# Performance work log

Measured on AMD Instinct MI355X. Metric: run time of the kernel, lower is better.

The kernel has to match this reference:

```python
import jax, jax.numpy as jnp
import numpy as np

N_NODES = 100000
N_EDGES = 1600000
IN_DIM, HID_DIM, OUT_DIM = 128, 128, 64


def setup_inputs() -> dict:
    key = jax.random.key(0)
    ks = jax.random.split(key, 8)
    x = jax.random.normal(ks[0], (N_NODES, IN_DIM), dtype=jnp.float32)
    edge_index = jax.random.randint(ks[1], (2, N_EDGES), 0, N_NODES, dtype=jnp.int64)
    s1 = 1.0 / np.sqrt(IN_DIM)
    s2 = 1.0 / np.sqrt(HID_DIM)
    return {
        "x": x,
        "edge_index": edge_index,
        "W1l": jax.random.normal(ks[2], (IN_DIM, HID_DIM), dtype=jnp.float32) * s1,
        "b1": jnp.zeros((HID_DIM,), dtype=jnp.float32),
        "W1r": jax.random.normal(ks[3], (IN_DIM, HID_DIM), dtype=jnp.float32) * s1,
        "W2l": jax.random.normal(ks[4], (HID_DIM, OUT_DIM), dtype=jnp.float32) * s2,
        "b2": jnp.zeros((OUT_DIM,), dtype=jnp.float32),
        "W2r": jax.random.normal(ks[5], (HID_DIM, OUT_DIM), dtype=jnp.float32) * s2,
    }


def _sage_conv(h, src, dst, n_nodes, Wl, bl, Wr):
    # mean-aggregate neighbor messages src -> dst, then linear + root linear
    msg = h[src]                                               # [E, d]
    summed = jax.ops.segment_sum(msg, dst, num_segments=n_nodes)
    cnt = jax.ops.segment_sum(jnp.ones((src.shape[0],), h.dtype), dst,
                              num_segments=n_nodes)
    aggr = summed / jnp.maximum(cnt, 1.0)[:, None]             # [N, d]
    return aggr @ Wl + bl + h @ Wr                             # [N, d_out]


def reference(x, edge_index, W1l, b1, W1r, W2l, b2, W2r):
    src, dst = edge_index[0], edge_index[1]
    n = x.shape[0]
    h = jax.nn.relu(_sage_conv(x, src, dst, n, W1l, b1, W1r))
    # dropout is identity in eval mode (training=False)
    return _sage_conv(h, src, dst, n, W2l, b2, W2r)
```

## Files before the change

### kernel.cpp

```cpp
#include <hip/hip_runtime.h>
#include <hip/hip_bf16.h>
#include <stdint.h>

#define N_NODES 100000
#define N_EDGES 1600000
#define IN_DIM 128
#define HID_DIM 128
#define OUT_DIM 64
#define NBUCKET 391
#define NBE 391
#define ECHUNK 4096
#define HM (NBUCKET * NBE)
#define NB_SCAN 150
#define SENTINEL N_NODES
#define PCAP 6144
#define GEMM_ROWBLKS 782

typedef __bf16 bf16x8 __attribute__((ext_vector_type(8)));
typedef float f32x4 __attribute__((ext_vector_type(4)));
typedef float f32x2 __attribute__((ext_vector_type(2)));

__device__ __forceinline__ uint16_t f_to_bf16(float f) {
    uint32_t u = __float_as_uint(f);
    u += 0x7fffu + ((u >> 16) & 1u);
    return (uint16_t)(u >> 16);
}
__device__ __forceinline__ uint32_t pack_bf16x2(float lo, float hi) {
    return (uint32_t)f_to_bf16(lo) | ((uint32_t)f_to_bf16(hi) << 16);
}


__global__ __launch_bounds__(256) void prep_k(const int* __restrict__ dst,
                                              const float* __restrict__ x,
                                              const float* __restrict__ W1l,
                                              const float* __restrict__ W1r,
                                              const float* __restrict__ W2l,
                                              const float* __restrict__ W2r,
                                              int* __restrict__ hist,
                                              uint32_t* __restrict__ xf8,
                                              uint16_t* __restrict__ wT1,
                                              uint16_t* __restrict__ wT2) {
    __shared__ int lh[NBUCKET];
    int blk = blockIdx.x, t = threadIdx.x;
    if (blk < NBE) {
        for (int i = t; i < NBUCKET; i += 256) lh[i] = 0;
        __syncthreads();
        int e0 = blk * ECHUNK;
        int e1 = e0 + ECHUNK; if (e1 > N_EDGES) e1 = N_EDGES;
        for (int e = e0 + t; e < e1; e += 256) atomicAdd(&lh[dst[e] >> 8], 1);
        __syncthreads();
        for (int i = t; i < NBUCKET; i += 256) hist[i * NBE + blk] = lh[i];
    } else if (blk < NBE + 6250) {
        int i = (blk - NBE) * 256 + t;
        if (blk == NBE && t < 32) xf8[N_NODES * 32 + t] = 0u;
        if (i >= N_NODES * IN_DIM / 8) return;
        const float4* xv = (const float4*)x;
        float4 v0 = xv[2 * i], v1 = xv[2 * i + 1];
        int p0 = __builtin_amdgcn_cvt_pk_fp8_f32(v0.x, v0.y, 0, false);
        p0 = __builtin_amdgcn_cvt_pk_fp8_f32(v0.z, v0.w, p0, true);
        int p1 = __builtin_amdgcn_cvt_pk_fp8_f32(v1.x, v1.y, 0, false);
        p1 = __builtin_amdgcn_cvt_pk_fp8_f32(v1.z, v1.w, p1, true);
        uint2 w2; w2.x = (uint32_t)p0; w2.y = (uint32_t)p1;
        ((uint2*)xf8)[i] = w2;
    } else {
        int i = (blk - NBE - 6250) * 256 + t;
        if (i < 128 * 256) {
            int n = i >> 8, k = i & 255;
            float v = (k < 128) ? W1l[k * 128 + n] : W1r[(k - 128) * 128 + n];
            wT1[i] = f_to_bf16(v);
        } else {
            int j = i - 128 * 256;
            if (j < 128 * 128) {
                int n = j >> 7, k = j & 127;
                float v = (n < 64) ? W2l[k * 64 + n] : W2r[k * 64 + (n - 64)];
                wT2[j] = f_to_bf16(v);
            }
        }
    }
}


__global__ void scan1_k(int* __restrict__ data, int* __restrict__ partials, int n) {
    __shared__ int sm[256];
    int tid = threadIdx.x;
    int base = blockIdx.x * 1024 + tid * 4;
    int v0 = 0, v1 = 0, v2 = 0, v3 = 0;
    if (base + 0 < n) v0 = data[base + 0];
    if (base + 1 < n) v1 = data[base + 1];
    if (base + 2 < n) v2 = data[base + 2];
    if (base + 3 < n) v3 = data[base + 3];
    int tot = v0 + v1 + v2 + v3;
    sm[tid] = tot;
    __syncthreads();
    int val = tot;
    for (int off = 1; off < 256; off <<= 1) {
        int x = (tid >= off) ? sm[tid - off] : 0;
        __syncthreads();
        val += x;
        sm[tid] = val;
        __syncthreads();
    }
    int excl = val - tot;
    if (tid == 255) partials[blockIdx.x] = val;
    if (base + 0 < n) data[base + 0] = excl;
    if (base + 1 < n) data[base + 1] = excl + v0;
    if (base + 2 < n) data[base + 2] = excl + v0 + v1;
    if (base + 3 < n) data[base + 3] = excl + v0 + v1 + v2;
}

__global__ void scan3_k(int* __restrict__ data, const int* __restrict__ partials, int n) {
    __shared__ int sm[256];
    __shared__ int sp[256];
    int t = threadIdx.x;
    int v = (t < NB_SCAN) ? partials[t] : 0;
    sm[t] = v;
    __syncthreads();
    int val = v;
    for (int off = 1; off < 256; off <<= 1) {
        int x = (t >= off) ? sm[t - off] : 0;
        __syncthreads();
        val += x;
        sm[t] = val;
        __syncthreads();
    }
    sp[t] = val - v;
    __syncthreads();
    int i = blockIdx.x * 256 + t;
    if (i < n) data[i] += sp[i >> 10];
}

__global__ __launch_bounds__(256) void scatter2_k(const int* __restrict__ src,
                                                  const int* __restrict__ dst,
                                                  const int* __restrict__ hoff,
                                                  uint32_t* __restrict__ packed) {
    __shared__ int loff[NBUCKET];
    int blk = blockIdx.x, t = threadIdx.x;
    for (int i = t; i < NBUCKET; i += 256) loff[i] = hoff[i * NBE + blk];
    __syncthreads();
    int e0 = blk * ECHUNK;
    int e1 = e0 + ECHUNK; if (e1 > N_EDGES) e1 = N_EDGES;
    for (int e = e0 + t; e < e1; e += 256) {
        int d = dst[e];
        int pos = atomicAdd(&loff[d >> 8], 1);
        packed[pos] = ((uint32_t)src[e] << 8) | (uint32_t)(d & 255);
    }
}


__global__ __launch_bounds__(256) void finalize_k(const uint32_t* __restrict__ packed,
                                                  const int* __restrict__ hoff,
                                                  int* __restrict__ csr,
                                                  int* __restrict__ deg,
                                                  int* __restrict__ prowst) {
    __shared__ int lhist[256];
    __shared__ int ssc[256];
    __shared__ int lcur[256];
    __shared__ int s_pcnt;
    __shared__ uint32_t lpk[PCAP];
    __shared__ int lcsr[PCAP];
    int b = blockIdx.x, t = threadIdx.x;
    int base = hoff[b * NBE];
    int next = (b + 1 < NBUCKET) ? hoff[(b + 1) * NBE] : N_EDGES;
    int cnt = next - base;
    lhist[t] = 0;
    __syncthreads();
    bool fit = (cnt <= PCAP);
    if (fit) {
        for (int i = t; i < cnt; i += 256) {
            uint32_t pk = packed[base + i];
            lpk[i] = pk;
            atomicAdd(&lhist[pk & 255u], 1);
        }
    } else {
        for (int i = t; i < cnt; i += 256) atomicAdd(&lhist[packed[base + i] & 255u], 1);
    }
    __syncthreads();
    int d = lhist[t];
    int pd = (d + 7) & ~7;
    ssc[t] = pd;
    __syncthreads();
    int val = pd;
    for (int off = 1; off < 256; off <<= 1) {
        int x = (t >= off) ? ssc[t - off] : 0;
        __syncthreads();
        val += x;
        ssc[t] = val;
        __syncthreads();
    }
    int excl = val - pd;
    lcur[t] = excl;
    if (t == 255) s_pcnt = val;
    int node = (b << 8) + t;
    if (node < N_NODES) { deg[node] = d; prowst[node] = b * PCAP + excl; }
    __syncthreads();
    int pcnt = s_pcnt;
    int cbase = b * PCAP;
    if (fit && pcnt <= PCAP) {
        for (int i = t; i < pcnt; i += 256) lcsr[i] = SENTINEL;
        __syncthreads();
        for (int i = t; i < cnt; i += 256) {
            uint32_t pk = lpk[i];
            int pos = atomicAdd(&lcur[pk & 255u], 1);
            lcsr[pos] = (int)(pk >> 8);
        }
        __syncthreads();
        for (int i = t; i < pcnt; i += 256) csr[cbase + i] = lcsr[i];
    } else {
        int lim = pcnt < PCAP ? pcnt : PCAP;
        for (int i = t; i < lim; i += 256) csr[cbase + i] = SENTINEL;
        __syncthreads();
        for (int i = t; i < cnt; i += 256) {
            uint32_t pk = packed[base + i];
            int pos = atomicAdd(&lcur[pk & 255u], 1);
            if (pos < PCAP) csr[cbase + pos] = (int)(pk >> 8);
        }
    }
}


__global__ void aggregate_k(const int* __restrict__ csr, const int* __restrict__ prowst,
                            const int* __restrict__ deg,
                            const uint32_t* __restrict__ inf8, uint32_t* __restrict__ out2) {
    int gw = (blockIdx.x * blockDim.x + threadIdx.x) >> 6;
    int lane = threadIdx.x & 63;
    int c = lane & 31, p = lane >> 5;
    int node = 2 * gw + p;
    int start = prowst[node];
    int d = deg[node];
    int pd = (d + 7) & ~7;
    f32x2 s01 = (f32x2){0.f, 0.f}, s23 = (f32x2){0.f, 0.f};
    for (int j = 0; j < pd; j += 8) {
        uint32_t q[8];
#pragma unroll
        for (int u = 0; u < 8; u++) {
            int s = csr[start + j + u];
            q[u] = inf8[(s << 5) + c];
        }
#pragma unroll
        for (int u = 0; u < 8; u++) {
            s01 += __builtin_amdgcn_cvt_pk_f32_fp8((int)q[u], false);
            s23 += __builtin_amdgcn_cvt_pk_f32_fp8((int)q[u], true);
        }
    }
    float inv = 1.0f / (float)(d > 0 ? d : 1);
    uint2 o;
    o.x = pack_bf16x2(s01[0] * inv, s01[1] * inv);
    o.y = pack_bf16x2(s23[0] * inv, s23[1] * inv);
    ((uint2*)out2)[node * 32 + c] = o;
}


__global__ __launch_bounds__(256, 2) void gemm12_k(const uint16_t* __restrict__ ab,
                                                   const float* __restrict__ x,
                                                   const uint16_t* __restrict__ wT1,
                                                   const float* __restrict__ b1,
                                                   const uint16_t* __restrict__ wT2,
                                                   const float* __restrict__ b2,
                                                   uint8_t* __restrict__ g,
                                                   float* __restrict__ z) {
    __shared__ uint16_t lwA[64 * 256];
    __shared__ uint16_t lhb[128 * 128];
    int t = threadIdx.x;
    int rowblk = blockIdx.x;
    if (rowblk == 0 && t < 16)
        ((uint32_t*)(g + (size_t)N_NODES * 64))[t] = 0u;

    int wave = t >> 6;
    int lane = t & 63;
    int m0 = rowblk * 128 + wave * 32;
    int mr = lane & 15, quad = lane >> 4;

    const uint16_t* A1[2];
    const float* A2[2];
#pragma unroll
    for (int s = 0; s < 2; s++) {
        int row = m0 + s * 16 + mr;
        if (row > N_NODES - 1) row = N_NODES - 1;
        A1[s] = ab + (size_t)row * 128 + quad * 8;
        A2[s] = x + (size_t)row * 128 + quad * 8;
    }

    for (int nh = 0; nh < 2; nh++) {
        {
            const uint4* gsrc = (const uint4*)wT1;
            uint4* ldst = (uint4*)lwA;
            for (int i = t; i < 2048; i += 256) {
                int r = i >> 5, cc = i & 31;
                ldst[(r << 5) + (cc ^ (r & 31))] = gsrc[((nh * 64 + r) << 5) + cc];
            }
        }
        __syncthreads();

        f32x4 acc[4][2];
#pragma unroll
        for (int nt = 0; nt < 4; nt++)
#pragma unroll
            for (int s = 0; s < 2; s++) acc[nt][s] = (f32x4){0.f, 0.f, 0.f, 0.f};

#pragma unroll
        for (int kt = 0; kt < 8; kt++) {
            bf16x8 av[2];
#pragma unroll
            for (int s = 0; s < 2; s++) {
                if (kt < 4) {
                    av[s] = *reinterpret_cast<const bf16x8*>(A1[s] + kt * 32);
                } else {
                    const float* ap = A2[s] + (kt - 4) * 32;
                    float4 f0 = *reinterpret_cast<const float4*>(ap);
                    float4 f1 = *reinterpret_cast<const float4*>(ap + 4);
                    union { uint16_t u[8]; bf16x8 v; } cv;
                    cv.u[0] = f_to_bf16(f0.x); cv.u[1] = f_to_bf16(f0.y);
                    cv.u[2] = f_to_bf16(f0.z); cv.u[3] = f_to_bf16(f0.w);
                    cv.u[4] = f_to_bf16(f1.x); cv.u[5] = f_to_bf16(f1.y);
                    cv.u[6] = f_to_bf16(f1.z); cv.u[7] = f_to_bf16(f1.w);
                    av[s] = cv.v;
                }
            }
#pragma unroll
            for (int nt = 0; nt < 4; nt++) {
                int brow = nt * 16 + mr;
                int chunk = kt * 4 + quad;
                const uint16_t* bp = lwA + (brow << 8) + ((chunk ^ (brow & 31)) << 3);
                bf16x8 b = *reinterpret_cast<const bf16x8*>(bp);
#pragma unroll
                for (int s = 0; s < 2; s++)
                    acc[nt][s] = __builtin_amdgcn_mfma_f32_16x16x32_bf16(av[s], b, acc[nt][s], 0, 0, 0);
            }
        }
        __syncthreads();

#pragma unroll
        for (int nt = 0; nt < 4; nt++) {
            int col = nh * 64 + nt * 16 + mr;
            float bias = b1[col];
            int c2 = col >> 3, clo = col & 7;
#pragma unroll
            for (int s = 0; s < 2; s++) {
#pragma unroll
                for (int r = 0; r < 4; r++) {
                    int lrow = wave * 32 + s * 16 + quad * 4 + r;
                    float v = acc[nt][s][r] + bias;
                    v = v > 0.f ? v : 0.f;
                    lhb[(lrow << 7) + ((c2 ^ (lrow & 15)) << 3) + clo] = f_to_bf16(v);
                }
            }
        }
    }

    {
        const uint4* gsrc = (const uint4*)wT2;
        uint4* ldst = (uint4*)lwA;
        for (int i = t; i < 2048; i += 256) {
            int r = i >> 4, cc = i & 15;
            ldst[(r << 4) + (cc ^ (r & 15))] = gsrc[(r << 4) + cc];
        }
    }
    __syncthreads();

    f32x4 acc2[8][2];
#pragma unroll
    for (int nt = 0; nt < 8; nt++)
#pragma unroll
        for (int s = 0; s < 2; s++) acc2[nt][s] = (f32x4){0.f, 0.f, 0.f, 0.f};

#pragma unroll
    for (int kt = 0; kt < 4; kt++) {
        bf16x8 av[2];
#pragma unroll
        for (int s = 0; s < 2; s++) {
            int row = wave * 32 + s * 16 + mr;
            int chunk = kt * 4 + quad;
            const uint16_t* ap = lhb + (row << 7) + ((chunk ^ (row & 15)) << 3);
            av[s] = *reinterpret_cast<const bf16x8*>(ap);
        }
#pragma unroll
        for (int nt = 0; nt < 8; nt++) {
            int brow = nt * 16 + mr;
            int chunk = kt * 4 + quad;
            const uint16_t* bp = lwA + (brow << 7) + ((chunk ^ (brow & 15)) << 3);
            bf16x8 b = *reinterpret_cast<const bf16x8*>(bp);
#pragma unroll
            for (int s = 0; s < 2; s++)
                acc2[nt][s] = __builtin_amdgcn_mfma_f32_16x16x32_bf16(av[s], b, acc2[nt][s], 0, 0, 0);
        }
    }

#pragma unroll
    for (int nt = 4; nt < 8; nt++) {
        int zcol = nt * 16 + mr - 64;
        float bias = b2[zcol];
#pragma unroll
        for (int s = 0; s < 2; s++) {
#pragma unroll
            for (int r = 0; r < 4; r++) {
                int row = m0 + s * 16 + quad * 4 + r;
                if (row < N_NODES)
                    z[(size_t)row * 64 + zcol] = acc2[nt][s][r] + bias;
            }
        }
    }
    __syncthreads();
    {
        uint8_t* ep8 = (uint8_t*)lwA;
#pragma unroll
        for (int nt = 0; nt < 4; nt++) {
            int col = nt * 16 + mr;
#pragma unroll
            for (int s = 0; s < 2; s++) {
#pragma unroll
                for (int r = 0; r < 4; r++) {
                    int lrow = wave * 32 + s * 16 + quad * 4 + r;
                    float v = acc2[nt][s][r];
                    int pk = __builtin_amdgcn_cvt_pk_fp8_f32(v, v, 0, false);
                    ep8[lrow * 80 + col] = (uint8_t)(pk & 0xff);
                }
            }
        }
        __syncthreads();
        int rows0 = rowblk * 128;
        for (int c2 = t; c2 < 512; c2 += 256) {
            int r = c2 >> 2, part = c2 & 3;
            int grow = rows0 + r;
            if (grow < N_NODES) {
                uint4 v = *reinterpret_cast<const uint4*>(ep8 + r * 80 + part * 16);
                *reinterpret_cast<uint4*>(g + (size_t)grow * 64 + part * 16) = v;
            }
        }
    }
}


__global__ void agg2_k(const int* __restrict__ csr, const int* __restrict__ prowst,
                       const int* __restrict__ deg,
                       const uint32_t* __restrict__ g4, const float* __restrict__ z,
                       float* __restrict__ out) {
    int gw = (blockIdx.x * blockDim.x + threadIdx.x) >> 6;
    int lane = threadIdx.x & 63;
    int c = lane & 15, q4 = lane >> 4;
    int node = 4 * gw + q4;
    int start = prowst[node];
    int d = deg[node];
    int pd = (d + 7) & ~7;
    f32x2 s01 = (f32x2){0.f, 0.f}, s23 = (f32x2){0.f, 0.f};
    for (int j = 0; j < pd; j += 8) {
        uint32_t q[8];
#pragma unroll
        for (int u = 0; u < 8; u++) {
            int s = csr[start + j + u];
            q[u] = g4[(s << 4) + c];
        }
#pragma unroll
        for (int u = 0; u < 8; u++) {
            s01 += __builtin_amdgcn_cvt_pk_f32_fp8((int)q[u], false);
            s23 += __builtin_amdgcn_cvt_pk_f32_fp8((int)q[u], true);
        }
    }
    float inv = 1.0f / (float)(d > 0 ? d : 1);
    float4 zz = ((const float4*)z)[node * 16 + c];
    float4 o;
    o.x = s01[0] * inv + zz.x;
    o.y = s01[1] * inv + zz.y;
    o.z = s23[0] * inv + zz.z;
    o.w = s23[1] * inv + zz.w;
    ((float4*)out)[node * 16 + c] = o;
}


extern "C" void kernel_launch(void* const* d_in, const int* in_sizes, int n_in,
                              void* d_out, int out_size, void* d_ws, size_t ws_size,
                              hipStream_t stream) {
    const float* x   = (const float*)d_in[0];
    const int*  ei   = (const int*)d_in[1];
    const float* W1l = (const float*)d_in[2];
    const float* b1  = (const float*)d_in[3];
    const float* W1r = (const float*)d_in[4];
    const float* W2l = (const float*)d_in[5];
    const float* b2  = (const float*)d_in[6];
    const float* W2r = (const float*)d_in[7];
    float* out = (float*)d_out;

    const int* srcv = ei;
    const int* dstv = ei + N_EDGES;

    char* ws = (char*)d_ws;
    int*      deg      = (int*)(ws + 0);
    int*      prowst   = (int*)(ws + 401408);
    int*      partials = (int*)(ws + 802816);
    int*      csr      = (int*)(ws + 1209344);
    uint16_t* wT1      = (uint16_t*)(ws + 13809664);
    uint16_t* wT2      = (uint16_t*)(ws + 13875200);
    uint8_t*  g        = (uint8_t*)(ws + 13907968);
    char*     abreg    = (ws + 39507968);
    uint16_t* ab       = (uint16_t*)abreg;
    float*    z        = (float*)abreg;
    uint32_t* packed   = (uint32_t*)(ws + 65107968);
    int*      hoff     = (int*)(ws + 65107968 + 6400000);
    uint32_t* xf8      = (uint32_t*)(ws + 65107968 + 7013376);

    prep_k<<<NBE + 6250 + 192, 256, 0, stream>>>(dstv, x, W1l, W1r, W2l, W2r,
                                                 hoff, xf8, wT1, wT2);
    scan1_k<<<NB_SCAN, 256, 0, stream>>>(hoff, partials, HM);
    scan3_k<<<(HM + 255) / 256, 256, 0, stream>>>(hoff, partials, HM);
    scatter2_k<<<NBE, 256, 0, stream>>>(srcv, dstv, hoff, packed);
    finalize_k<<<NBUCKET, 256, 0, stream>>>(packed, hoff, csr, deg, prowst);

    aggregate_k<<<12500, 256, 0, stream>>>(csr, prowst, deg, xf8, (uint32_t*)ab);
    gemm12_k<<<GEMM_ROWBLKS, 256, 0, stream>>>(ab, x, wT1, b1, wT2, b2, g, z);
    agg2_k<<<6250, 256, 0, stream>>>(csr, prowst, deg, (const uint32_t*)g, z, out);
}
```

Baseline: 153.4 us.

## Fuse layer-1 neighbor aggregation into the GEMM kernel

Removes the separate aggregate kernel and computes the mean-aggregated fp8 neighbor features directly inside gemm12_k, with each lane accumulating the MFMA A-fragment slices it needs in registers. This avoids writing and re-reading the bf16 aggregate buffer and saves one launch. In exchange, the gather now runs with only 782 blocks, each lane serially walking one node's neighbor list and doing strided 8-byte loads. The launch bounds also raise register pressure, so latency hiding may be worse than in the dedicated kernel.

```diff
diff --git a/kernel.cpp b/kernel.cpp
--- a/kernel.cpp
+++ b/kernel.cpp
@@ -218,39 +218,10 @@
 }
 
 
-__global__ void aggregate_k(const int* __restrict__ csr, const int* __restrict__ prowst,
-                            const int* __restrict__ deg,
-                            const uint32_t* __restrict__ inf8, uint32_t* __restrict__ out2) {
-    int gw = (blockIdx.x * blockDim.x + threadIdx.x) >> 6;
-    int lane = threadIdx.x & 63;
-    int c = lane & 31, p = lane >> 5;
-    int node = 2 * gw + p;
-    int start = prowst[node];
-    int d = deg[node];
-    int pd = (d + 7) & ~7;
-    f32x2 s01 = (f32x2){0.f, 0.f}, s23 = (f32x2){0.f, 0.f};
-    for (int j = 0; j < pd; j += 8) {
-        uint32_t q[8];
-#pragma unroll
-        for (int u = 0; u < 8; u++) {
-            int s = csr[start + j + u];
-            q[u] = inf8[(s << 5) + c];
-        }
-#pragma unroll
-        for (int u = 0; u < 8; u++) {
-            s01 += __builtin_amdgcn_cvt_pk_f32_fp8((int)q[u], false);
-            s23 += __builtin_amdgcn_cvt_pk_f32_fp8((int)q[u], true);
-        }
-    }
-    float inv = 1.0f / (float)(d > 0 ? d : 1);
-    uint2 o;
-    o.x = pack_bf16x2(s01[0] * inv, s01[1] * inv);
-    o.y = pack_bf16x2(s23[0] * inv, s23[1] * inv);
-    ((uint2*)out2)[node * 32 + c] = o;
-}
-
-
-__global__ __launch_bounds__(256, 2) void gemm12_k(const uint16_t* __restrict__ ab,
+__global__ __launch_bounds__(256, 2) void gemm12_k(const int* __restrict__ csr,
+                                                   const int* __restrict__ prowst,
+                                                   const int* __restrict__ deg,
+                                                   const uint32_t* __restrict__ xf8,
                                                    const float* __restrict__ x,
                                                    const uint16_t* __restrict__ wT1,
                                                    const float* __restrict__ b1,
@@ -270,14 +241,53 @@
     int m0 = rowblk * 128 + wave * 32;
     int mr = lane & 15, quad = lane >> 4;
 
-    const uint16_t* A1[2];
     const float* A2[2];
 #pragma unroll
     for (int s = 0; s < 2; s++) {
         int row = m0 + s * 16 + mr;
         if (row > N_NODES - 1) row = N_NODES - 1;
-        A1[s] = ab + (size_t)row * 128 + quad * 8;
         A2[s] = x + (size_t)row * 128 + quad * 8;
+    }
+
+    bf16x8 a1[2][4];
+#pragma unroll
+    for (int s = 0; s < 2; s++) {
+        int row = m0 + s * 16 + mr;
+        if (row > N_NODES - 1) row = N_NODES - 1;
+        int start = prowst[row];
+        int d = deg[row];
+        int pd = (d + 7) & ~7;
+        f32x2 agg[4][4];
+#pragma unroll
+        for (int m = 0; m < 4; m++)
+#pragma unroll
+            for (int p = 0; p < 4; p++) agg[m][p] = (f32x2){0.f, 0.f};
+        for (int j = 0; j < pd; j += 4) {
+            int sr[4];
+#pragma unroll
+            for (int u = 0; u < 4; u++) sr[u] = csr[start + j + u];
+#pragma unroll
+            for (int u = 0; u < 4; u++) {
+                const uint2* xr = (const uint2*)(xf8 + ((size_t)sr[u] << 5));
+#pragma unroll
+                for (int m = 0; m < 4; m++) {
+                    uint2 w = xr[quad + 4 * m];
+                    agg[m][0] += __builtin_amdgcn_cvt_pk_f32_fp8((int)w.x, false);
+                    agg[m][1] += __builtin_amdgcn_cvt_pk_f32_fp8((int)w.x, true);
+                    agg[m][2] += __builtin_amdgcn_cvt_pk_f32_fp8((int)w.y, false);
+                    agg[m][3] += __builtin_amdgcn_cvt_pk_f32_fp8((int)w.y, true);
+                }
+            }
+        }
+        float inv = 1.0f / (float)(d > 0 ? d : 1);
+#pragma unroll
+        for (int m = 0; m < 4; m++) {
+            union { uint32_t w[4]; bf16x8 v; } cv;
+#pragma unroll
+            for (int p = 0; p < 4; p++)
+                cv.w[p] = pack_bf16x2(agg[m][p][0] * inv, agg[m][p][1] * inv);
+            a1[s][m] = cv.v;
+        }
     }
 
     for (int nh = 0; nh < 2; nh++) {
@@ -303,7 +313,7 @@
 #pragma unroll
             for (int s = 0; s < 2; s++) {
                 if (kt < 4) {
-                    av[s] = *reinterpret_cast<const bf16x8*>(A1[s] + kt * 32);
+                    av[s] = a1[s][kt];
                 } else {
                     const float* ap = A2[s] + (kt - 4) * 32;
                     float4 f0 = *reinterpret_cast<const float4*>(ap);
@@ -490,9 +500,7 @@
     uint16_t* wT1      = (uint16_t*)(ws + 13809664);
     uint16_t* wT2      = (uint16_t*)(ws + 13875200);
     uint8_t*  g        = (uint8_t*)(ws + 13907968);
-    char*     abreg    = (ws + 39507968);
-    uint16_t* ab       = (uint16_t*)abreg;
-    float*    z        = (float*)abreg;
+    float*    z        = (float*)(ws + 39507968);
     uint32_t* packed   = (uint32_t*)(ws + 65107968);
     int*      hoff     = (int*)(ws + 65107968 + 6400000);
     uint32_t* xf8      = (uint32_t*)(ws + 65107968 + 7013376);
@@ -504,7 +512,7 @@
     scatter2_k<<<NBE, 256, 0, stream>>>(srcv, dstv, hoff, packed);
     finalize_k<<<NBUCKET, 256, 0, stream>>>(packed, hoff, csr, deg, prowst);
 
-    aggregate_k<<<12500, 256, 0, stream>>>(csr, prowst, deg, xf8, (uint32_t*)ab);
-    gemm12_k<<<GEMM_ROWBLKS, 256, 0, stream>>>(ab, x, wT1, b1, wT2, b2, g, z);
+    gemm12_k<<<GEMM_ROWBLKS, 256, 0, stream>>>(csr, prowst, deg, xf8, x,
+                                               wT1, b1, wT2, b2, g, z);
     agg2_k<<<6250, 256, 0, stream>>>(csr, prowst, deg, (const uint32_t*)g, z, out);
 }
```

After: 189.2 us. +23.4%, slower.
